# Kernel optimization log

Hardware: AMD Instinct MI355X
Metric: run time of the kernel (lower is better)

Reference implementation:

```python
import jax, jax.numpy as jnp
import numpy as np

B, L, C = 8, 1024, 1024
H, DK = 16, 64
E, HID = 16, 64
CAP_FACTOR = 0.5
EPS = 1e-5


def setup_inputs() -> dict:
    key = jax.random.key(0)
    ks = jax.random.split(key, 20)
    f32 = jnp.float32
    s_c = 1.0 / np.sqrt(C)
    s_h = 1.0 / np.sqrt(HID)
    inp = {
        "qx": jax.random.normal(ks[0], (B, L, C), f32),
        "kx": jax.random.normal(ks[1], (B, L, C), f32),
        "vx": jax.random.normal(ks[2], (B, L, C), f32),
        "maskPAD": jnp.ones((B, L), dtype=bool),
        # attention params (torch Linear weight layout [out,in])
        "WQ": jax.random.normal(ks[3], (H * DK, C), f32) * s_c,
        "bQ": jnp.zeros((H * DK,), f32),
        "WK": jax.random.normal(ks[4], (H * DK, C), f32) * s_c,
        "bK": jnp.zeros((H * DK,), f32),
        "WV": jax.random.normal(ks[5], (H * DK, C), f32) * s_c,
        "bV": jnp.zeros((H * DK,), f32),
        "WO": jax.random.normal(ks[6], (C, H * DK), f32) * s_c,
        "bO": jnp.zeros((C,), f32),
        "ln1_w": jnp.ones((C,), f32),
        "ln1_b": jnp.zeros((C,), f32),
        # router
        "Wsw": jax.random.normal(ks[7], (E, C), f32) * s_c,
        "bsw": jnp.zeros((E,), f32),
        # per-expert FFN: Linear(C,HID) -> ReLU -> Linear(HID,C)
        "W1": jax.random.normal(ks[8], (E, C, HID), f32) * s_c,
        "b1": jnp.zeros((E, HID), f32),
        "W2": jax.random.normal(ks[9], (E, HID, C), f32) * s_h,
        "b2": jnp.zeros((E, C), f32),
    }
    return inp


def _layernorm(x, w, b):
    mu = jnp.mean(x, axis=-1, keepdims=True)
    var = jnp.mean(jnp.square(x - mu), axis=-1, keepdims=True)
    return (x - mu) * jax.lax.rsqrt(var + EPS) * w + b


def _moe(x2d, Wsw, bsw, W1, b1, W2, b2):
    # x2d: [N, C] tokens; top-1 switch routing with capacity-based token dropping
    N = x2d.shape[0]
    cap = int(CAP_FACTOR * N / E)
    logits = x2d @ Wsw.T + bsw                      # [N, E]
    probs = jax.nn.softmax(logits, axis=-1)
    routes = jnp.argmax(probs, axis=-1)             # [N]
    pmax = jnp.max(probs, axis=-1)                  # [N]
    onehot = jax.nn.one_hot(routes, E, dtype=jnp.int32)
    # position of each token within its expert's queue (deterministic order;
    # torch uses randperm before dropping -- math identical up to permutation)
    pos = jnp.take_along_axis(jnp.cumsum(onehot, axis=0) - 1, routes[:, None], axis=1)[:, 0]
    kept = pos < cap
    slot = jnp.where(kept, routes * cap + pos, E * cap)  # dropped -> trash slot
    buf = jnp.zeros((E * cap + 1, x2d.shape[1]), x2d.dtype).at[slot].set(x2d)
    eb = buf[: E * cap].reshape(E, cap, -1)         # [E, cap, C]
    h = jax.nn.relu(jnp.einsum("ecd,edh->ech", eb, W1) + b1[:, None, :])
    y = jnp.einsum("ech,ehd->ecd", h, W2) + b2[:, None, :]
    yflat = y.reshape(E * cap, -1)
    gathered = yflat[jnp.where(kept, routes * cap + pos, 0)]
    final = jnp.where(kept[:, None], gathered, x2d)  # dropped tokens pass through
    # is_scale_prob=False: multiply by p/stop_grad(p) (==1 in fwd, grads flow)
    scale = pmax / jax.lax.stop_gradient(pmax)
    return final * scale[:, None]


def reference(qx, kx, vx, maskPAD, WQ, bQ, WK, bK, WV, bV, WO, bO,
              ln1_w, ln1_b, Wsw, bsw, W1, b1, W2, b2):
    # multi-head attention (maskPAD is unused in the original SelfAttention_1)
    q = (qx @ WQ.T + bQ).reshape(B, L, H, DK)
    k = (kx @ WK.T + bK).reshape(B, L, H, DK)
    v = (vx @ WV.T + bV).reshape(B, L, H, DK)
    scores = jnp.einsum("bqhd,bkhd->bhqk", q, k) / np.sqrt(DK).astype(np.float32)
    alpha = jax.nn.softmax(scores, axis=-1)
    z = jnp.einsum("bhqk,bkhd->bqhd", alpha, v).reshape(B, L, H * DK)
    att = z @ WO.T + bO
    zn = _layernorm(qx + att, ln1_w, ln1_b)          # norm1 residual
    moe_out = _moe(zn.reshape(B * L, C), Wsw, bsw, W1, b1, W2, b2).reshape(B, L, C)
    out = zn + moe_out                               # note: norm2 unused in original
    return (out, kx, vx, maskPAD)
```

## Files before the change

kernel.cpp:

```cpp
#include <hip/hip_runtime.h>


typedef __bf16 bf16;
typedef __bf16 bf16x4 __attribute__((ext_vector_type(4)));
typedef __bf16 bf16x8 __attribute__((ext_vector_type(8)));
typedef float  f32x4  __attribute__((ext_vector_type(4)));

#define NB    8
#define LL    1024
#define CC    1024
#define NH    16
#define DKD   64
#define NE    16
#define NHID  64
#define CAP   256
#define NTOK  (NB*LL)
#define MB    (1024*1024)

__device__ __forceinline__ void gload16(const bf16* g, bf16* l)
{
    __builtin_amdgcn_global_load_lds(
        (const __attribute__((address_space(1))) void*)g,
        (__attribute__((address_space(3))) void*)l, 16, 0, 0);
}

__device__ inline void split3v(const f32x4 v, bf16x4& a, bf16x4& b, bf16x4& c)
{
#pragma unroll
    for (int k = 0; k < 4; k++) {
        const float x  = v[k];
        const bf16  hi = (bf16)x;
        const float r1 = x - (float)hi;
        const bf16  md = (bf16)r1;
        const float r2 = r1 - (float)md;
        a[k] = hi; b[k] = md; c[k] = (bf16)r2;
    }
}

__device__ inline bf16x8 pack8(const bf16x4 a, const bf16x4 b)
{
    bf16x8 r;
#pragma unroll
    for (int e = 0; e < 4; e++) { r[e] = a[e]; r[4 + e] = b[e]; }
    return r;
}

__global__ __launch_bounds__(256)
void split3(const float* __restrict__ z, bf16* __restrict__ z1,
            bf16* __restrict__ z2, bf16* __restrict__ z3)
{
    const size_t i = ((size_t)blockIdx.x * 256 + threadIdx.x) * 4;
    const f32x4 v = *(const f32x4*)(z + i);
    bf16x4 a, b, c;
    split3v(v, a, b, c);
    *(bf16x4*)(z1 + i) = a;
    *(bf16x4*)(z2 + i) = b;
    *(bf16x4*)(z3 + i) = c;
}

__global__ __launch_bounds__(256)
void gemm_limb6(const bf16* __restrict__ A0, const bf16* __restrict__ A1,
                const bf16* __restrict__ A2,
                const bf16* __restrict__ W0, const bf16* __restrict__ W1l,
                const bf16* __restrict__ W2l,
                const float* __restrict__ bias, float* __restrict__ C,
                int M, int N, int K)
{
    __shared__ __align__(16) bf16 As[3][128][32];
    __shared__ __align__(16) bf16 Ws[3][128][32];

    const int tid  = threadIdx.x;
    const int lane = tid & 63;
    const int wv   = tid >> 6;
    const int bm = blockIdx.x * 128;
    const int bn = blockIdx.y * 128;
    const int wm = (wv & 1) * 64;
    const int wn = (wv >> 1) * 64;
    const int lr = lane & 15;
    const int lq = lane >> 4;

    const int r0  = tid >> 2;
    const int cc8 = (tid & 3) * 8;

    const bf16* Aps[3] = {A0, A1, A2};
    const bf16* Wps[3] = {W0, W1l, W2l};

    f32x4 acc[4][4];
#pragma unroll
    for (int i = 0; i < 4; i++)
#pragma unroll
        for (int j = 0; j < 4; j++) acc[i][j] = f32x4{0.f, 0.f, 0.f, 0.f};

    constexpr int PI[6] = {0, 0, 1, 1, 0, 2};
    constexpr int PJ[6] = {0, 1, 0, 1, 2, 0};

    for (int k0 = 0; k0 < K; k0 += 32) {
#pragma unroll
        for (int l = 0; l < 3; l++) {
            const bf16* ga = Aps[l] + (size_t)(bm + r0) * K + k0 + cc8;
            const bf16* gw = Wps[l] + (size_t)(bn + r0) * K + k0 + cc8;
            gload16(ga,                  &As[l][r0][cc8]);
            gload16(ga + (size_t)64 * K, &As[l][r0 + 64][cc8]);
            gload16(gw,                  &Ws[l][r0][cc8]);
            gload16(gw + (size_t)64 * K, &Ws[l][r0 + 64][cc8]);
        }
        __syncthreads();

        bf16x8 af[3][4], bfr[3][4];
#pragma unroll
        for (int i = 0; i < 4; i++) {
            af[0][i] = *(const bf16x8*)&As[0][wm + i * 16 + lr][lq * 8];
            af[1][i] = *(const bf16x8*)&As[1][wm + i * 16 + lr][lq * 8];
            af[2][i] = *(const bf16x8*)&As[2][wm + i * 16 + lr][lq * 8];
        }
#pragma unroll
        for (int j = 0; j < 4; j++) {
            bfr[0][j] = *(const bf16x8*)&Ws[0][wn + j * 16 + lr][lq * 8];
            bfr[1][j] = *(const bf16x8*)&Ws[1][wn + j * 16 + lr][lq * 8];
            bfr[2][j] = *(const bf16x8*)&Ws[2][wn + j * 16 + lr][lq * 8];
        }
#pragma unroll
        for (int p = 0; p < 6; p++)
#pragma unroll
            for (int i = 0; i < 4; i++)
#pragma unroll
                for (int j = 0; j < 4; j++)
                    acc[i][j] = __builtin_amdgcn_mfma_f32_16x16x32_bf16(
                        af[PI[p]][i], bfr[PJ[p]][j], acc[i][j], 0, 0, 0);
        __syncthreads();
    }
#pragma unroll
    for (int i = 0; i < 4; i++)
#pragma unroll
        for (int j = 0; j < 4; j++) {
            const int col = bn + wn + j * 16 + lr;
            const float bv = bias[col];
#pragma unroll
            for (int r = 0; r < 4; r++) {
                const int row = bm + wm + i * 16 + lq * 4 + r;
                C[(size_t)row * N + col] = acc[i][j][r] + bv;
            }
        }
}

__global__ __launch_bounds__(256)
void vsplit(const float* __restrict__ Vf, bf16* __restrict__ T0,
            bf16* __restrict__ T1, bf16* __restrict__ T2)
{
    __shared__ __align__(16) bf16 Lt[3][64][72];
    const int tid = threadIdx.x;
    const int bh  = blockIdx.x;
    const int b   = bh >> 4, h = bh & 15;
    const int l0  = blockIdx.y * 64;

    const int dql = tid & 15;
    const int lrr = tid >> 4;
#pragma unroll
    for (int p = 0; p < 4; p++) {
        const int l = p * 16 + lrr;
        const f32x4 v = *(const f32x4*)(
            Vf + (size_t)(b * LL + l0 + l) * 1024 + h * 64 + dql * 4);
        bf16x4 a, bq, c; split3v(v, a, bq, c);
#pragma unroll
        for (int e = 0; e < 4; e++) {
            Lt[0][dql * 4 + e][l] = a[e];
            Lt[1][dql * 4 + e][l] = bq[e];
            Lt[2][dql * 4 + e][l] = c[e];
        }
    }
    __syncthreads();
    const int d  = tid >> 2;
    const int lc = tid & 3;
    const size_t o = (size_t)bh * 65536 + (size_t)d * 1024 + l0 + lc * 16;
    *(bf16x8*)(T0 + o)     = *(const bf16x8*)&Lt[0][d][lc * 16];
    *(bf16x8*)(T0 + o + 8) = *(const bf16x8*)&Lt[0][d][lc * 16 + 8];
    *(bf16x8*)(T1 + o)     = *(const bf16x8*)&Lt[1][d][lc * 16];
    *(bf16x8*)(T1 + o + 8) = *(const bf16x8*)&Lt[1][d][lc * 16 + 8];
    *(bf16x8*)(T2 + o)     = *(const bf16x8*)&Lt[2][d][lc * 16];
    *(bf16x8*)(T2 + o + 8) = *(const bf16x8*)&Lt[2][d][lc * 16 + 8];
}

__global__ __launch_bounds__(256)
void flash_mfma(float* __restrict__ Qf, const float* __restrict__ Kf,
                const bf16* __restrict__ Vt0, const bf16* __restrict__ Vt1,
                const bf16* __restrict__ Vt2)
{
    __shared__ __align__(16) bf16  Ks[3][32][64];
    __shared__ __align__(16) bf16  Vs[3][64][32];
    __shared__ __align__(16) float Ps[128][32];

    const int tid  = threadIdx.x;
    const int lane = tid & 63;
    const int w    = tid >> 6;
    const int lr   = lane & 15;
    const int lq   = lane >> 4;
    const int lr7  = lr & 7;

    const int bid = (int)blockIdx.x;
    const int qb  = (bid >> 3) & 7;
    const int bh  = (bid & 7) * 16 + (bid >> 6);
    const int b   = bh >> 4, h = bh & 15;
    const int q0  = qb * 128;
    const size_t base = (size_t)b * LL * 1024 + (size_t)h * 64;

    bf16x8 qf[3][2][2];
#pragma unroll
    for (int mi = 0; mi < 2; mi++)
#pragma unroll
        for (int ks = 0; ks < 2; ks++) {
            const float* src = Qf + base +
                (size_t)(q0 + w * 32 + mi * 16 + lr) * 1024 + ks * 32 + lq * 8;
            f32x4 v0 = *(const f32x4*)src;
            f32x4 v1 = *(const f32x4*)(src + 4);
            v0 *= 0.125f; v1 *= 0.125f;
            bf16x4 a0, b0, c0, a1, b1, c1;
            split3v(v0, a0, b0, c0);
            split3v(v1, a1, b1, c1);
            qf[0][mi][ks] = pack8(a0, a1);
            qf[1][mi][ks] = pack8(b0, b1);
            qf[2][mi][ks] = pack8(c0, c1);
        }

    bf16x8 onesf;
#pragma unroll
    for (int e = 0; e < 8; e++) onesf[e] = (bf16)1.0f;

    const int kr  = tid >> 3, kq = tid & 7;
    const int kpg = kq ^ (kr & 7);
    const int vr  = tid >> 2, vg = tid & 3;
    const int vlg = vg ^ ((vr >> 1) & 3);
    const float* kbase = Kf + base + (size_t)kr * 1024 + kq * 8;
    const size_t vtb = (size_t)bh * 65536 + (size_t)vr * 1024 + (size_t)vlg * 8;

    f32x4  kp0 = *(const f32x4*)(kbase);
    f32x4  kp1 = *(const f32x4*)(kbase + 4);
    bf16x8 vp0 = *(const bf16x8*)(Vt0 + vtb);
    bf16x8 vp1 = *(const bf16x8*)(Vt1 + vtb);
    bf16x8 vp2 = *(const bf16x8*)(Vt2 + vtb);

    f32x4 acc_l[2];
    f32x4 accO[2][4];
#pragma unroll
    for (int mi = 0; mi < 2; mi++) {
        acc_l[mi] = f32x4{0.f, 0.f, 0.f, 0.f};
#pragma unroll
        for (int nd = 0; nd < 4; nd++) accO[mi][nd] = f32x4{0.f, 0.f, 0.f, 0.f};
    }

    constexpr int PI[6] = {0, 0, 1, 1, 0, 2};
    constexpr int PJ[6] = {0, 1, 0, 1, 2, 0};

    for (int kt = 0; kt < 32; kt++) {
        __syncthreads();
        {
            bf16x4 a0, b0, c0, a1, b1, c1;
            split3v(kp0, a0, b0, c0);
            split3v(kp1, a1, b1, c1);
            *(bf16x8*)&Ks[0][kr][kpg * 8] = pack8(a0, a1);
            *(bf16x8*)&Ks[1][kr][kpg * 8] = pack8(b0, b1);
            *(bf16x8*)&Ks[2][kr][kpg * 8] = pack8(c0, c1);
            *(bf16x8*)&Vs[0][vr][vg * 8] = vp0;
            *(bf16x8*)&Vs[1][vr][vg * 8] = vp1;
            *(bf16x8*)&Vs[2][vr][vg * 8] = vp2;
        }
        __syncthreads();
        if (kt < 31) {
            const float* ks_ = kbase + (size_t)(kt + 1) * 32 * 1024;
            kp0 = *(const f32x4*)ks_;
            kp1 = *(const f32x4*)(ks_ + 4);
            const size_t vo = vtb + (size_t)(kt + 1) * 32;
            vp0 = *(const bf16x8*)(Vt0 + vo);
            vp1 = *(const bf16x8*)(Vt1 + vo);
            vp2 = *(const bf16x8*)(Vt2 + vo);
        }

        f32x4 accS[2][2];
#pragma unroll
        for (int mi = 0; mi < 2; mi++)
#pragma unroll
            for (int nj = 0; nj < 2; nj++) accS[mi][nj] = f32x4{0.f, 0.f, 0.f, 0.f};
#pragma unroll
        for (int nj = 0; nj < 2; nj++) {
            bf16x8 kfr[3][2];
#pragma unroll
            for (int ks = 0; ks < 2; ks++) {
                const int kg = (ks * 4 + lq) ^ lr7;
                kfr[0][ks] = *(const bf16x8*)&Ks[0][nj * 16 + lr][kg * 8];
                kfr[1][ks] = *(const bf16x8*)&Ks[1][nj * 16 + lr][kg * 8];
                kfr[2][ks] = *(const bf16x8*)&Ks[2][nj * 16 + lr][kg * 8];
            }
#pragma unroll
            for (int p = 0; p < 6; p++)
#pragma unroll
                for (int mi = 0; mi < 2; mi++)
#pragma unroll
                    for (int ks = 0; ks < 2; ks++)
                        accS[mi][nj] = __builtin_amdgcn_mfma_f32_16x16x32_bf16(
                            qf[PI[p]][mi][ks], kfr[PJ[p]][ks], accS[mi][nj], 0, 0, 0);
        }

#pragma unroll
        for (int mi = 0; mi < 2; mi++)
#pragma unroll
            for (int rr = 0; rr < 4; rr++) {
                const float p0 = __expf(accS[mi][0][rr]);
                const float p1 = __expf(accS[mi][1][rr]);
                const int prow = w * 32 + mi * 16 + lq * 4 + rr;
                const int pr7  = prow & 7;
                Ps[prow][(((lr >> 2) ^ pr7) << 2) | (lr & 3)]       = p0;
                Ps[prow][(((4 + (lr >> 2)) ^ pr7) << 2) | (lr & 3)] = p1;
            }

        bf16x8 pf[3][2];
#pragma unroll
        for (int mi = 0; mi < 2; mi++) {
            const int row = w * 32 + mi * 16 + lr;
            const f32x4 v0 = *(const f32x4*)&Ps[row][((2 * lq) ^ lr7) * 4];
            const f32x4 v1 = *(const f32x4*)&Ps[row][((2 * lq + 1) ^ lr7) * 4];
            bf16x4 a0, b0, c0, a1, b1, c1;
            split3v(v0, a0, b0, c0);
            split3v(v1, a1, b1, c1);
            pf[0][mi] = pack8(a0, a1);
            pf[1][mi] = pack8(b0, b1);
            pf[2][mi] = pack8(c0, c1);
        }

#pragma unroll
        for (int mi = 0; mi < 2; mi++) {
            acc_l[mi] = __builtin_amdgcn_mfma_f32_16x16x32_bf16(
                pf[0][mi], onesf, acc_l[mi], 0, 0, 0);
            acc_l[mi] = __builtin_amdgcn_mfma_f32_16x16x32_bf16(
                pf[1][mi], onesf, acc_l[mi], 0, 0, 0);
            acc_l[mi] = __builtin_amdgcn_mfma_f32_16x16x32_bf16(
                pf[2][mi], onesf, acc_l[mi], 0, 0, 0);
        }

        const int vgp = lq ^ ((lr >> 1) & 3);
#pragma unroll
        for (int nd = 0; nd < 4; nd++) {
            bf16x8 vfr[3];
            vfr[0] = *(const bf16x8*)&Vs[0][nd * 16 + lr][vgp * 8];
            vfr[1] = *(const bf16x8*)&Vs[1][nd * 16 + lr][vgp * 8];
            vfr[2] = *(const bf16x8*)&Vs[2][nd * 16 + lr][vgp * 8];
#pragma unroll
            for (int p = 0; p < 6; p++)
#pragma unroll
                for (int mi = 0; mi < 2; mi++)
                    accO[mi][nd] = __builtin_amdgcn_mfma_f32_16x16x32_bf16(
                        pf[PI[p]][mi], vfr[PJ[p]], accO[mi][nd], 0, 0, 0);
        }
    }

#pragma unroll
    for (int mi = 0; mi < 2; mi++) {
        float inv[4];
#pragma unroll
        for (int rr = 0; rr < 4; rr++) inv[rr] = 1.f / acc_l[mi][rr];
#pragma unroll
        for (int nd = 0; nd < 4; nd++)
#pragma unroll
            for (int rr = 0; rr < 4; rr++)
                Qf[base + (size_t)(q0 + w * 32 + mi * 16 + lq * 4 + rr) * 1024 +
                   nd * 16 + lr] = accO[mi][nd][rr] * inv[rr];
    }
}

__global__ __launch_bounds__(256)
void ln_kernel(const float* __restrict__ qx, const float* __restrict__ att,
               const float* __restrict__ w, const float* __restrict__ bch,
               float* __restrict__ zn)
{
    const int row = blockIdx.x, tid = threadIdx.x;
    const size_t off = (size_t)row * 1024 + tid * 4;
    const f32x4 q4 = *(const f32x4*)(qx + off);
    const f32x4 a4 = *(const f32x4*)(att + off);
    float x[4];
#pragma unroll
    for (int i = 0; i < 4; i++) x[i] = q4[i] + a4[i];

    __shared__ float red[8];
    float part = x[0] + x[1] + x[2] + x[3];
#pragma unroll
    for (int d = 1; d < 64; d <<= 1) part += __shfl_xor(part, d);
    if ((tid & 63) == 0) red[tid >> 6] = part;
    __syncthreads();
    const float mu = (red[0] + red[1] + red[2] + red[3]) * (1.f / 1024.f);

    float p2 = 0.f;
#pragma unroll
    for (int i = 0; i < 4; i++) { const float d = x[i] - mu; p2 += d * d; }
#pragma unroll
    for (int d = 1; d < 64; d <<= 1) p2 += __shfl_xor(p2, d);
    if ((tid & 63) == 0) red[4 + (tid >> 6)] = p2;
    __syncthreads();
    const float var  = (red[4] + red[5] + red[6] + red[7]) * (1.f / 1024.f);
    const float rstd = 1.f / sqrtf(var + 1e-5f);

    const f32x4 w4 = *(const f32x4*)(w + tid * 4);
    const f32x4 b4 = *(const f32x4*)(bch + tid * 4);
    f32x4 out;
#pragma unroll
    for (int i = 0; i < 4; i++)
        out[i] = (x[i] - mu) * rstd * w4[i] + b4[i];
    *(f32x4*)(zn + off) = out;
}

__global__ __launch_bounds__(64)
void router_kernel(const float* __restrict__ zn, const float* __restrict__ Wsw,
                   const float* __restrict__ bsw, int* __restrict__ routes)
{
    const int t = blockIdx.x, lane = threadIdx.x;
    const float* x = zn + (size_t)t * 1024;
    float acc[16];
#pragma unroll
    for (int e = 0; e < 16; e++) acc[e] = 0.f;
    for (int ii = 0; ii < 16; ii++) {
        const float xv = x[lane + 64 * ii];
#pragma unroll
        for (int e = 0; e < 16; e++)
            acc[e] += xv * Wsw[e * 1024 + lane + 64 * ii];
    }
#pragma unroll
    for (int e = 0; e < 16; e++)
#pragma unroll
        for (int d = 1; d < 64; d <<= 1) acc[e] += __shfl_xor(acc[e], d);
    if (lane == 0) {
        float best = acc[0] + bsw[0];
        int bi = 0;
#pragma unroll
        for (int e = 1; e < 16; e++) {
            const float lg = acc[e] + bsw[e];
            if (lg > best) { best = lg; bi = e; }
        }
        routes[t] = bi;
    }
}

__global__ __launch_bounds__(1024)
void route_scan(const int* __restrict__ routes, int* __restrict__ slot_of_token,
                int* __restrict__ token_of_slot)
{
    const int wv = threadIdx.x >> 6;
    const int lane = threadIdx.x & 63;
    int cnt = 0;
    for (int c = 0; c < NTOK / 64; c++) {
        const int tok = c * 64 + lane;
        const bool match = (routes[tok] == wv);
        const unsigned long long mask = __ballot(match);
        const int pos = cnt + __popcll(mask & ((1ull << lane) - 1ull));
        if (match) {
            if (pos < CAP) {
                slot_of_token[tok] = wv * CAP + pos;
                token_of_slot[wv * CAP + pos] = tok;
            } else slot_of_token[tok] = -1;
        }
        cnt += __popcll(mask);
    }
    const int filled = cnt < CAP ? cnt : CAP;
    for (int s2 = filled + lane; s2 < CAP; s2 += 64)
        token_of_slot[wv * CAP + s2] = -1;
}

__global__ __launch_bounds__(64)
void ffn1(const float* __restrict__ zn, const int* __restrict__ token_of_slot,
          const float* __restrict__ W1, const float* __restrict__ b1,
          float* __restrict__ hbuf)
{
    const int s = blockIdx.x, lane = threadIdx.x;
    const int tok = token_of_slot[s];
    if (tok < 0) return;
    const int e = s >> 8;
    const float* w = W1 + (size_t)e * CC * NHID + lane;
    const float* x = zn + (size_t)tok * 1024;
    float acc = 0.f;
#pragma unroll 8
    for (int i = 0; i < 1024; i++) acc += x[i] * w[(size_t)i * NHID];
    acc += b1[e * NHID + lane];
    hbuf[(size_t)s * NHID + lane] = fmaxf(acc, 0.f);
}

__global__ __launch_bounds__(256)
void ffn2(const float* __restrict__ hbuf, const int* __restrict__ token_of_slot,
          const float* __restrict__ W2, const float* __restrict__ b2,
          float* __restrict__ ybuf)
{
    const int s = blockIdx.x, tid = threadIdx.x;
    const int tok = token_of_slot[s];
    if (tok < 0) return;
    const int e = s >> 8;
    const int c0 = tid * 4;
    const float* w = W2 + (size_t)e * NHID * CC + c0;
    const float* hrow = hbuf + (size_t)s * NHID;
    const f32x4 b4 = *(const f32x4*)(b2 + e * CC + c0);
    float a0 = b4[0], a1 = b4[1], a2 = b4[2], a3 = b4[3];
#pragma unroll 8
    for (int k = 0; k < NHID; k++) {
        const float hv = hrow[k];
        const f32x4 w4 = *(const f32x4*)(w + (size_t)k * CC);
        a0 += hv * w4[0]; a1 += hv * w4[1];
        a2 += hv * w4[2]; a3 += hv * w4[3];
    }
    const f32x4 out = {a0, a1, a2, a3};
    *(f32x4*)(ybuf + (size_t)s * 1024 + c0) = out;
}

__global__ __launch_bounds__(256)
void assemble(const float* __restrict__ zn, const float* __restrict__ ybuf,
              const int* __restrict__ slot_of_token, float* __restrict__ out)
{
    const int tok = blockIdx.x, tid = threadIdx.x;
    const int slot = slot_of_token[tok];
    const size_t off = (size_t)tok * 1024 + tid * 4;
    const f32x4 z4 = *(const f32x4*)(zn + off);
    f32x4 m4;
    if (slot >= 0) m4 = *(const f32x4*)(ybuf + (size_t)slot * 1024 + tid * 4);
    else           m4 = z4;
    f32x4 o;
#pragma unroll
    for (int i = 0; i < 4; i++) o[i] = z4[i] + m4[i];
    *(f32x4*)(out + off) = o;
}

__global__ __launch_bounds__(256)
void fill_mask(float* __restrict__ p, int n)
{
    const int i = blockIdx.x * 256 + threadIdx.x;
    if (i < n) p[i] = 1.0f;
}

extern "C" void kernel_launch(void* const* d_in, const int* in_sizes, int n_in,
                              void* d_out, int out_size, void* d_ws, size_t ws_size,
                              hipStream_t stream)
{
    (void)out_size; (void)ws_size;
    const float* qx = (const float*)d_in[0];
    const float* kx = (const float*)d_in[1];
    const float* vx = (const float*)d_in[2];
    int wbase = 4;
    if (n_in >= 4 && in_sizes[3] != NB * LL) wbase = 3;
    const float* WQ   = (const float*)d_in[wbase + 0];
    const float* bQ   = (const float*)d_in[wbase + 1];
    const float* WK   = (const float*)d_in[wbase + 2];
    const float* bK   = (const float*)d_in[wbase + 3];
    const float* WV   = (const float*)d_in[wbase + 4];
    const float* bV   = (const float*)d_in[wbase + 5];
    const float* WO   = (const float*)d_in[wbase + 6];
    const float* bO   = (const float*)d_in[wbase + 7];
    const float* ln1w = (const float*)d_in[wbase + 8];
    const float* ln1b = (const float*)d_in[wbase + 9];
    const float* Wsw  = (const float*)d_in[wbase + 10];
    const float* bsw  = (const float*)d_in[wbase + 11];
    const float* W1   = (const float*)d_in[wbase + 12];
    const float* b1   = (const float*)d_in[wbase + 13];
    const float* W2   = (const float*)d_in[wbase + 14];
    const float* b2   = (const float*)d_in[wbase + 15];

    char* D   = (char*)d_out;
    char* wsb = (char*)d_ws;

    float* Qbuf = (float*)(wsb);
    bf16*  la0  = (bf16*)(D);
    bf16*  la1  = (bf16*)(D + (size_t)16 * MB);
    bf16*  la2  = (bf16*)(wsb + (size_t)32 * MB);
    bf16*  lw0  = (bf16*)(wsb + (size_t)48 * MB);
    bf16*  lw1  = (bf16*)(wsb + (size_t)50 * MB);
    bf16*  lw2  = (bf16*)(wsb + (size_t)52 * MB);
    float* Kbuf = (float*)(D + (size_t)32 * MB);
    float* Vbuf = (float*)(D + (size_t)64 * MB);

    const dim3 gblk(NTOK / 128, CC / 128, 1);
    const int GA = NTOK * 1024 / 1024;
    const int GW = CC * 1024 / 1024;

    split3<<<GA, 256, 0, stream>>>(qx, la0, la1, la2);
    split3<<<GW, 256, 0, stream>>>(WQ, lw0, lw1, lw2);
    gemm_limb6<<<gblk, 256, 0, stream>>>(la0, la1, la2, lw0, lw1, lw2, bQ, Qbuf, NTOK, CC, CC);
    split3<<<GA, 256, 0, stream>>>(kx, la0, la1, la2);
    split3<<<GW, 256, 0, stream>>>(WK, lw0, lw1, lw2);
    gemm_limb6<<<gblk, 256, 0, stream>>>(la0, la1, la2, lw0, lw1, lw2, bK, Kbuf, NTOK, CC, CC);
    split3<<<GA, 256, 0, stream>>>(vx, la0, la1, la2);
    split3<<<GW, 256, 0, stream>>>(WV, lw0, lw1, lw2);
    gemm_limb6<<<gblk, 256, 0, stream>>>(la0, la1, la2, lw0, lw1, lw2, bV, Vbuf, NTOK, CC, CC);

    bf16* Vt0 = la0;
    bf16* Vt1 = la1;
    bf16* Vt2 = la2;
    vsplit<<<dim3(128, 16), 256, 0, stream>>>(Vbuf, Vt0, Vt1, Vt2);

    flash_mfma<<<1024, 256, 0, stream>>>(Qbuf, Kbuf, Vt0, Vt1, Vt2);

    split3<<<GA, 256, 0, stream>>>(Qbuf, la0, la1, la2);
    split3<<<GW, 256, 0, stream>>>(WO, lw0, lw1, lw2);
    float* attbuf = Kbuf;
    gemm_limb6<<<gblk, 256, 0, stream>>>(la0, la1, la2, lw0, lw1, lw2, bO, attbuf, NTOK, CC, CC);

    float* znbuf = Vbuf;
    ln_kernel<<<NTOK, 256, 0, stream>>>(qx, attbuf, ln1w, ln1b, znbuf);

    int*   routes        = (int*)(wsb + (size_t)32 * MB);
    int*   slot_of_token = (int*)(wsb + (size_t)32 * MB + 64 * 1024);
    int*   token_of_slot = (int*)(wsb + (size_t)32 * MB + 128 * 1024);
    float* hbuf          = (float*)(wsb + (size_t)33 * MB);
    float* ybuf          = (float*)(wsb + (size_t)34 * MB);

    router_kernel<<<NTOK, 64, 0, stream>>>(znbuf, Wsw, bsw, routes);
    route_scan<<<1, 1024, 0, stream>>>(routes, slot_of_token, token_of_slot);
    ffn1<<<NE * CAP, 64, 0, stream>>>(znbuf, token_of_slot, W1, b1, hbuf);
    ffn2<<<NE * CAP, 256, 0, stream>>>(hbuf, token_of_slot, W2, b2, ybuf);

    assemble<<<NTOK, 256, 0, stream>>>(znbuf, ybuf, slot_of_token, (float*)d_out);

    hipMemcpyAsync(D + (size_t)32 * MB, (const void*)kx,
                   (size_t)NTOK * 1024 * 4, hipMemcpyDeviceToDevice, stream);
    hipMemcpyAsync(D + (size_t)64 * MB, (const void*)vx,
                   (size_t)NTOK * 1024 * 4, hipMemcpyDeviceToDevice, stream);
    fill_mask<<<NTOK / 256, 256, 0, stream>>>((float*)d_out + (size_t)3 * NTOK * 1024, NTOK);
}
```

Before: 997.8 us.

## Double-buffer flash K/V tiles, batch 8 slots per FFN block, fold mask fill

The flash attention kernel now keeps two shared-memory buffers for its K/V tiles, alternated each iteration, so the barrier at the top of the loop can be removed. The expert FFN kernels each process 8 slots per block instead of one, so every weight element loaded is reused across 8 tokens, and dropped slots are skipped only at the final store. The separate mask-fill kernel is folded into the assemble kernel to save a launch. The cost is twice the LDS for K/V in flash, possibly lowering occupancy, plus more registers in the FFN kernels. Unused slots still do full compute.

```diff
diff --git a/kernel.cpp b/kernel.cpp
--- a/kernel.cpp
+++ b/kernel.cpp
@@ -185,8 +185,8 @@
                 const bf16* __restrict__ Vt0, const bf16* __restrict__ Vt1,
                 const bf16* __restrict__ Vt2)
 {
-    __shared__ __align__(16) bf16  Ks[3][32][64];
-    __shared__ __align__(16) bf16  Vs[3][64][32];
+    __shared__ __align__(16) bf16  Ks[2][3][32][64];
+    __shared__ __align__(16) bf16  Vs[2][3][64][32];
     __shared__ __align__(16) float Ps[128][32];
 
     const int tid  = threadIdx.x;
@@ -251,17 +251,17 @@
     constexpr int PJ[6] = {0, 1, 0, 1, 2, 0};
 
     for (int kt = 0; kt < 32; kt++) {
-        __syncthreads();
+        const int bs = kt & 1;
         {
             bf16x4 a0, b0, c0, a1, b1, c1;
             split3v(kp0, a0, b0, c0);
             split3v(kp1, a1, b1, c1);
-            *(bf16x8*)&Ks[0][kr][kpg * 8] = pack8(a0, a1);
-            *(bf16x8*)&Ks[1][kr][kpg * 8] = pack8(b0, b1);
-            *(bf16x8*)&Ks[2][kr][kpg * 8] = pack8(c0, c1);
-            *(bf16x8*)&Vs[0][vr][vg * 8] = vp0;
-            *(bf16x8*)&Vs[1][vr][vg * 8] = vp1;
-            *(bf16x8*)&Vs[2][vr][vg * 8] = vp2;
+            *(bf16x8*)&Ks[bs][0][kr][kpg * 8] = pack8(a0, a1);
+            *(bf16x8*)&Ks[bs][1][kr][kpg * 8] = pack8(b0, b1);
+            *(bf16x8*)&Ks[bs][2][kr][kpg * 8] = pack8(c0, c1);
+            *(bf16x8*)&Vs[bs][0][vr][vg * 8] = vp0;
+            *(bf16x8*)&Vs[bs][1][vr][vg * 8] = vp1;
+            *(bf16x8*)&Vs[bs][2][vr][vg * 8] = vp2;
         }
         __syncthreads();
         if (kt < 31) {
@@ -285,9 +285,9 @@
 #pragma unroll
             for (int ks = 0; ks < 2; ks++) {
                 const int kg = (ks * 4 + lq) ^ lr7;
-                kfr[0][ks] = *(const bf16x8*)&Ks[0][nj * 16 + lr][kg * 8];
-                kfr[1][ks] = *(const bf16x8*)&Ks[1][nj * 16 + lr][kg * 8];
-                kfr[2][ks] = *(const bf16x8*)&Ks[2][nj * 16 + lr][kg * 8];
+                kfr[0][ks] = *(const bf16x8*)&Ks[bs][0][nj * 16 + lr][kg * 8];
+                kfr[1][ks] = *(const bf16x8*)&Ks[bs][1][nj * 16 + lr][kg * 8];
+                kfr[2][ks] = *(const bf16x8*)&Ks[bs][2][nj * 16 + lr][kg * 8];
             }
 #pragma unroll
             for (int p = 0; p < 6; p++)
@@ -339,9 +339,9 @@
 #pragma unroll
         for (int nd = 0; nd < 4; nd++) {
             bf16x8 vfr[3];
-            vfr[0] = *(const bf16x8*)&Vs[0][nd * 16 + lr][vgp * 8];
-            vfr[1] = *(const bf16x8*)&Vs[1][nd * 16 + lr][vgp * 8];
-            vfr[2] = *(const bf16x8*)&Vs[2][nd * 16 + lr][vgp * 8];
+            vfr[0] = *(const bf16x8*)&Vs[bs][0][nd * 16 + lr][vgp * 8];
+            vfr[1] = *(const bf16x8*)&Vs[bs][1][nd * 16 + lr][vgp * 8];
+            vfr[2] = *(const bf16x8*)&Vs[bs][2][nd * 16 + lr][vgp * 8];
 #pragma unroll
             for (int p = 0; p < 6; p++)
 #pragma unroll
@@ -466,17 +466,29 @@
           const float* __restrict__ W1, const float* __restrict__ b1,
           float* __restrict__ hbuf)
 {
-    const int s = blockIdx.x, lane = threadIdx.x;
-    const int tok = token_of_slot[s];
-    if (tok < 0) return;
-    const int e = s >> 8;
+    const int s0 = blockIdx.x * 8, lane = threadIdx.x;
+    const int e = s0 >> 8;
+    int tk[8];
+    const float* xs[8];
+    float acc[8];
+#pragma unroll
+    for (int u = 0; u < 8; u++) {
+        tk[u] = token_of_slot[s0 + u];
+        xs[u] = zn + (size_t)(tk[u] < 0 ? 0 : tk[u]) * 1024;
+        acc[u] = 0.f;
+    }
     const float* w = W1 + (size_t)e * CC * NHID + lane;
-    const float* x = zn + (size_t)tok * 1024;
-    float acc = 0.f;
-#pragma unroll 8
-    for (int i = 0; i < 1024; i++) acc += x[i] * w[(size_t)i * NHID];
-    acc += b1[e * NHID + lane];
-    hbuf[(size_t)s * NHID + lane] = fmaxf(acc, 0.f);
+#pragma unroll 4
+    for (int i = 0; i < 1024; i++) {
+        const float wv = w[(size_t)i * NHID];
+#pragma unroll
+        for (int u = 0; u < 8; u++) acc[u] += xs[u][i] * wv;
+    }
+    const float bv = b1[e * NHID + lane];
+#pragma unroll
+    for (int u = 0; u < 8; u++)
+        if (tk[u] >= 0)
+            hbuf[(size_t)(s0 + u) * NHID + lane] = fmaxf(acc[u] + bv, 0.f);
 }
 
 __global__ __launch_bounds__(256)
@@ -484,29 +496,35 @@
           const float* __restrict__ W2, const float* __restrict__ b2,
           float* __restrict__ ybuf)
 {
-    const int s = blockIdx.x, tid = threadIdx.x;
-    const int tok = token_of_slot[s];
-    if (tok < 0) return;
-    const int e = s >> 8;
+    const int s0 = blockIdx.x * 8, tid = threadIdx.x;
+    const int e = s0 >> 8;
     const int c0 = tid * 4;
     const float* w = W2 + (size_t)e * NHID * CC + c0;
-    const float* hrow = hbuf + (size_t)s * NHID;
     const f32x4 b4 = *(const f32x4*)(b2 + e * CC + c0);
-    float a0 = b4[0], a1 = b4[1], a2 = b4[2], a3 = b4[3];
-#pragma unroll 8
+    int tk[8];
+    f32x4 a[8];
+#pragma unroll
+    for (int u = 0; u < 8; u++) { tk[u] = token_of_slot[s0 + u]; a[u] = b4; }
+#pragma unroll 4
     for (int k = 0; k < NHID; k++) {
-        const float hv = hrow[k];
         const f32x4 w4 = *(const f32x4*)(w + (size_t)k * CC);
-        a0 += hv * w4[0]; a1 += hv * w4[1];
-        a2 += hv * w4[2]; a3 += hv * w4[3];
-    }
-    const f32x4 out = {a0, a1, a2, a3};
-    *(f32x4*)(ybuf + (size_t)s * 1024 + c0) = out;
+#pragma unroll
+        for (int u = 0; u < 8; u++) {
+            const float hv = hbuf[(size_t)(s0 + u) * NHID + k];
+            a[u][0] += hv * w4[0]; a[u][1] += hv * w4[1];
+            a[u][2] += hv * w4[2]; a[u][3] += hv * w4[3];
+        }
+    }
+#pragma unroll
+    for (int u = 0; u < 8; u++)
+        if (tk[u] >= 0)
+            *(f32x4*)(ybuf + (size_t)(s0 + u) * 1024 + c0) = a[u];
 }
 
 __global__ __launch_bounds__(256)
 void assemble(const float* __restrict__ zn, const float* __restrict__ ybuf,
-              const int* __restrict__ slot_of_token, float* __restrict__ out)
+              const int* __restrict__ slot_of_token, float* __restrict__ out,
+              float* __restrict__ maskout)
 {
     const int tok = blockIdx.x, tid = threadIdx.x;
     const int slot = slot_of_token[tok];
@@ -519,13 +537,7 @@
 #pragma unroll
     for (int i = 0; i < 4; i++) o[i] = z4[i] + m4[i];
     *(f32x4*)(out + off) = o;
-}
-
-__global__ __launch_bounds__(256)
-void fill_mask(float* __restrict__ p, int n)
-{
-    const int i = blockIdx.x * 256 + threadIdx.x;
-    if (i < n) p[i] = 1.0f;
+    if (tid == 0) maskout[tok] = 1.0f;
 }
 
 extern "C" void kernel_launch(void* const* d_in, const int* in_sizes, int n_in,
@@ -605,14 +617,14 @@
 
     router_kernel<<<NTOK, 64, 0, stream>>>(znbuf, Wsw, bsw, routes);
     route_scan<<<1, 1024, 0, stream>>>(routes, slot_of_token, token_of_slot);
-    ffn1<<<NE * CAP, 64, 0, stream>>>(znbuf, token_of_slot, W1, b1, hbuf);
-    ffn2<<<NE * CAP, 256, 0, stream>>>(hbuf, token_of_slot, W2, b2, ybuf);
-
-    assemble<<<NTOK, 256, 0, stream>>>(znbuf, ybuf, slot_of_token, (float*)d_out);
+    ffn1<<<NE * CAP / 8, 64, 0, stream>>>(znbuf, token_of_slot, W1, b1, hbuf);
+    ffn2<<<NE * CAP / 8, 256, 0, stream>>>(hbuf, token_of_slot, W2, b2, ybuf);
+
+    assemble<<<NTOK, 256, 0, stream>>>(znbuf, ybuf, slot_of_token, (float*)d_out,
+                                       (float*)d_out + (size_t)3 * NTOK * 1024);
 
     hipMemcpyAsync(D + (size_t)32 * MB, (const void*)kx,
                    (size_t)NTOK * 1024 * 4, hipMemcpyDeviceToDevice, stream);
     hipMemcpyAsync(D + (size_t)64 * MB, (const void*)vx,
                    (size_t)NTOK * 1024 * 4, hipMemcpyDeviceToDevice, stream);
-    fill_mask<<<NTOK / 256, 256, 0, stream>>>((float*)d_out + (size_t)3 * NTOK * 1024, NTOK);
-}
+}
```

New measurement: 1.037 ms. +4.0%, slower.
